# Performance work log

Measured on AMD Instinct MI355X. Metric: run time of the kernel, lower is better.

Reference implementation:

```python
import jax, jax.numpy as jnp
import numpy as np

B, C, L = 4, 256, 4096
NUM_GROUPS = 32
EPS = 1e-6


def setup_inputs() -> dict:
    key = jax.random.key(0)
    ks = jax.random.split(key, 8)
    s = 1.0 / np.sqrt(C)  # conv1x1 init scale
    return {
        "x": jax.random.normal(ks[0], (B, C, L), dtype=jnp.float32),
        "norm_g": jnp.ones((C,), dtype=jnp.float32),
        "norm_b": jnp.zeros((C,), dtype=jnp.float32),
        "q_w": jax.random.normal(ks[1], (C, C), dtype=jnp.float32) * s,
        "q_b": jnp.zeros((C,), dtype=jnp.float32),
        "k_w": jax.random.normal(ks[2], (C, C), dtype=jnp.float32) * s,
        "k_b": jnp.zeros((C,), dtype=jnp.float32),
        "v_w": jax.random.normal(ks[3], (C, C), dtype=jnp.float32) * s,
        "v_b": jnp.zeros((C,), dtype=jnp.float32),
        "proj_w": jax.random.normal(ks[4], (C, C), dtype=jnp.float32) * s,
        "proj_b": jnp.zeros((C,), dtype=jnp.float32),
    }


def _group_norm(x, g, b):
    # x: [B, C, L] -> groups of C//NUM_GROUPS channels
    Bx, Cx, Lx = x.shape
    xg = x.reshape(Bx, NUM_GROUPS, Cx // NUM_GROUPS, Lx)
    mean = jnp.mean(xg, axis=(2, 3), keepdims=True)
    var = jnp.var(xg, axis=(2, 3), keepdims=True)
    xn = ((xg - mean) * jax.lax.rsqrt(var + EPS)).reshape(Bx, Cx, Lx)
    return xn * g[None, :, None] + b[None, :, None]


def _conv1x1(w, b, h):
    # w: [Cout, Cin], h: [B, Cin, L]
    return jnp.einsum("oc,bcl->bol", w, h) + b[None, :, None]


def reference(x, norm_g, norm_b, q_w, q_b, k_w, k_b, v_w, v_b, proj_w, proj_b):
    h = _group_norm(x, norm_g, norm_b)
    q = _conv1x1(q_w, q_b, h)   # [B, C, L]
    k = _conv1x1(k_w, k_b, h)
    v = _conv1x1(v_w, v_b, h)

    scale = jnp.asarray(x.shape[1], x.dtype) ** -0.5
    # w_[b,i,j] = sum_c q[b,c,i] * k[b,c,j]
    w_ = jnp.einsum("bci,bcj->bij", q, k) * scale
    w_ = jax.nn.softmax(w_, axis=2)
    # h_[b,c,i] = sum_j v[b,c,j] * w_[b,i,j]
    h2 = jnp.einsum("bcj,bij->bci", v, w_)

    out = _conv1x1(proj_w, proj_b, h2)
    return x + out
```

## Files before the change

### kernel.cpp

```cpp
#include <hip/hip_runtime.h>

#define B_ 4
#define C_ 256
#define L_ 4096
#define NG 32
#define CPG 8
#define BL (B_ * L_)
#define KPART 4
#define KEYS_PP (L_ / KPART)
#define QLOG2E 0.09016844f

typedef __attribute__((ext_vector_type(8))) __bf16 bf16x8;
typedef __attribute__((ext_vector_type(8))) short s16x8;
typedef __attribute__((ext_vector_type(4))) float f32x4;
typedef __attribute__((ext_vector_type(16))) float f32x16;

__device__ __forceinline__ unsigned short f2bf(float f) {
  unsigned int u = __builtin_bit_cast(unsigned int, f);
  u += 0x7fffu + ((u >> 16) & 1u);
  return (unsigned short)(u >> 16);
}
__device__ __forceinline__ float bf2f(unsigned short u) {
  unsigned int v = ((unsigned int)u) << 16;
  return __builtin_bit_cast(float, v);
}
#if __has_builtin(__builtin_amdgcn_exp2f)
#define EXP2F(x) __builtin_amdgcn_exp2f(x)
#else
#define EXP2F(x) exp2f(x)
#endif

__device__ __forceinline__ void gld_lds16(const void* g, void* l) {
  __builtin_amdgcn_global_load_lds(
      (const __attribute__((address_space(1))) unsigned int*)g,
      (__attribute__((address_space(3))) unsigned int*)l, 16, 0, 0);
}

__device__ __forceinline__ float red16_add(float x) {
  int i;
  i = __builtin_amdgcn_update_dpp(0, __builtin_bit_cast(int, x), 0xB1, 0xF, 0xF, false);
  x += __builtin_bit_cast(float, i);
  i = __builtin_amdgcn_update_dpp(0, __builtin_bit_cast(int, x), 0x4E, 0xF, 0xF, false);
  x += __builtin_bit_cast(float, i);
  i = __builtin_amdgcn_update_dpp(0, __builtin_bit_cast(int, x), 0x124, 0xF, 0xF, false);
  x += __builtin_bit_cast(float, i);
  i = __builtin_amdgcn_update_dpp(0, __builtin_bit_cast(int, x), 0x128, 0xF, 0xF, false);
  x += __builtin_bit_cast(float, i);
  return x;
}

__global__ __launch_bounds__(256) void init_k(const float* __restrict__ qw,
                                              const float* __restrict__ kw,
                                              const float* __restrict__ vw,
                                              const float* __restrict__ pw,
                                              const float* __restrict__ qb,
                                              const float* __restrict__ x,
                                              unsigned short* __restrict__ wq,
                                              unsigned short* __restrict__ wk,
                                              unsigned short* __restrict__ wv,
                                              unsigned short* __restrict__ wp,
                                              float* __restrict__ qbs,
                                              float* __restrict__ stats) {
  const int bid = blockIdx.x;
  const int t = threadIdx.x;
  if (bid < 128) {
    const int m = bid >> 5;
    const int blk = bid & 31;
    const float* src = (m == 0) ? qw : (m == 1) ? kw : (m == 2) ? vw : pw;
    unsigned short* dst = (m == 0) ? wq : (m == 1) ? wk : (m == 2) ? wv : wp;
    const float sc = (m == 0) ? QLOG2E : 1.0f;
    const int base = (blk * 256 + t) * 8;
    f32x4 a = *(const f32x4*)(src + base);
    f32x4 b = *(const f32x4*)(src + base + 4);
    s16x8 o;
#pragma unroll
    for (int j = 0; j < 4; ++j) {
      o[j] = (short)f2bf(a[j] * sc);
      o[4 + j] = (short)f2bf(b[j] * sc);
    }
    *(s16x8*)(dst + base) = o;
    if (m == 0 && blk == 0) qbs[t] = qb[t] * QLOG2E;
  } else {
    const int bg = bid - 128;
    const float* base = x + (size_t)bg * (CPG * L_);
    float s = 0.f, ss = 0.f;
#pragma unroll
    for (int i = 0; i < 32; ++i) {
      f32x4 v = *(const f32x4*)(base + (size_t)(t + i * 256) * 4);
#pragma unroll
      for (int j = 0; j < 4; ++j) { s += v[j]; ss += v[j] * v[j]; }
    }
#pragma unroll
    for (int d = 1; d < 64; d <<= 1) {
      s += __shfl_xor(s, d, 64);
      ss += __shfl_xor(ss, d, 64);
    }
    __shared__ float red[8];
    if ((t & 63) == 0) { red[(t >> 6) * 2] = s; red[(t >> 6) * 2 + 1] = ss; }
    __syncthreads();
    if (t == 0) {
      float S = red[0] + red[2] + red[4] + red[6];
      float SS = red[1] + red[3] + red[5] + red[7];
      const float inv_n = 1.f / (float)(CPG * L_);
      float mean = S * inv_n;
      float var = SS * inv_n - mean * mean;
      stats[bg * 2] = mean;
      stats[bg * 2 + 1] = rsqrtf(var + 1e-6f);
    }
  }
}

__global__ __launch_bounds__(256) void gn_apply_k(const float* __restrict__ x,
                                                  const float* __restrict__ stats,
                                                  const float* __restrict__ gam,
                                                  const float* __restrict__ bet,
                                                  unsigned short* __restrict__ ht) {
  __shared__ unsigned short tile[64 * 256];
  const int blk = blockIdx.x;
  const int b = blk >> 6;
  const int l0 = (blk & 63) * 64;
  const int t = threadIdx.x;
  const int c = t;
  const float mean = stats[(b * NG + (c >> 3)) * 2];
  const float rstd = stats[(b * NG + (c >> 3)) * 2 + 1];
  const float sc = rstd * gam[c];
  const float sb = bet[c] - mean * sc;
  const float* row = x + ((size_t)(b * C_ + c)) * L_ + l0;
#pragma unroll
  for (int v = 0; v < 16; ++v) {
    f32x4 f = *(const f32x4*)(row + v * 4);
#pragma unroll
    for (int j = 0; j < 4; ++j) tile[(v * 4 + j) * 256 + c] = f2bf(f[j] * sc + sb);
  }
  __syncthreads();
#pragma unroll
  for (int i = 0; i < 8; ++i) {
    int id = t + i * 256;
    int l = id >> 5, off = id & 31;
    *(s16x8*)(ht + ((size_t)(b * L_) + l0 + l) * 256 + off * 8) =
        *(const s16x8*)(tile + l * 256 + off * 8);
  }
}

__global__ __launch_bounds__(256) void gemm_t_k(const unsigned short* __restrict__ A,
                                                const unsigned short* __restrict__ W,
                                                const float* __restrict__ bias,
                                                unsigned short* __restrict__ Ct) {
  __shared__ unsigned short Al[64 * 256];
  __shared__ unsigned short Wl[64 * 256];
  const int m0 = blockIdx.x * 64;
  const int n0 = blockIdx.y * 64;
  const int t = threadIdx.x;
  const int w = t >> 6, lane = t & 63, l15 = lane & 15, q = lane >> 4;
#pragma unroll
  for (int i = 0; i < 8; ++i) {
    const int seg = w * 8 + i;
    const int idx = seg * 64 + lane;
    const int row = idx >> 5, c16 = idx & 31;
    gld_lds16(A + (size_t)(m0 + row) * 256 + ((c16 ^ (row & 7)) * 8), Al + seg * 512);
    gld_lds16(W + (size_t)(n0 + row) * 256 + ((c16 ^ (row & 7)) * 8), Wl + seg * 512);
  }
  __syncthreads();
  bf16x8 af[8];
#pragma unroll
  for (int kf = 0; kf < 8; ++kf) {
    int row = w * 16 + l15;
    af[kf] = *(const bf16x8*)(Al + row * 256 + (((kf * 4 + q) ^ (row & 7)) * 8));
  }
  f32x4 acc[4];
#pragma unroll
  for (int nf = 0; nf < 4; ++nf) {
    f32x4 cacc = {0.f, 0.f, 0.f, 0.f};
#pragma unroll
    for (int kf = 0; kf < 8; ++kf) {
      int row = nf * 16 + l15;
      bf16x8 bf = *(const bf16x8*)(Wl + row * 256 + (((kf * 4 + q) ^ (row & 7)) * 8));
      cacc = __builtin_amdgcn_mfma_f32_16x16x32_bf16(af[kf], bf, cacc, 0, 0, 0);
    }
    acc[nf] = cacc;
  }
#pragma unroll
  for (int nf = 0; nf < 4; ++nf) {
    const int n = n0 + nf * 16 + l15;
    const float bs = bias[n];
#pragma unroll
    for (int r = 0; r < 4; ++r) {
      const int m = m0 + w * 16 + q * 4 + r;
      Ct[(size_t)m * 256 + n] = f2bf(acc[nf][r] + bs);
    }
  }
}

template <int MODE>
__global__ __launch_bounds__(256) void gemm_n_k(const unsigned short* __restrict__ X,
                                                const unsigned short* __restrict__ W,
                                                const float* __restrict__ bias,
                                                const float* __restrict__ xres,
                                                void* __restrict__ outv) {
  __shared__ unsigned short Wl[64 * 256];
  __shared__ unsigned short Xl[64 * 256];
  const int i0 = blockIdx.x * 64;
  const int o0 = blockIdx.y * 64;
  const int b = blockIdx.z;
  const int t = threadIdx.x;
  const int w = t >> 6, lane = t & 63, l15 = lane & 15, q = lane >> 4;
#pragma unroll
  for (int i = 0; i < 8; ++i) {
    const int seg = w * 8 + i;
    const int idx = seg * 64 + lane;
    const int row = idx >> 5, c16 = idx & 31;
    gld_lds16(W + (size_t)(o0 + row) * 256 + ((c16 ^ (row & 7)) * 8), Wl + seg * 512);
    gld_lds16(X + ((size_t)(b * L_) + i0 + row) * 256 + ((c16 ^ (row & 7)) * 8),
              Xl + seg * 512);
  }
  __syncthreads();
  bf16x8 af[8];
#pragma unroll
  for (int kf = 0; kf < 8; ++kf) {
    int row = w * 16 + l15;
    af[kf] = *(const bf16x8*)(Wl + row * 256 + (((kf * 4 + q) ^ (row & 7)) * 8));
  }
  f32x4 acc[4];
#pragma unroll
  for (int nf = 0; nf < 4; ++nf) {
    f32x4 cacc = {0.f, 0.f, 0.f, 0.f};
#pragma unroll
    for (int kf = 0; kf < 8; ++kf) {
      int row = nf * 16 + l15;
      bf16x8 bf = *(const bf16x8*)(Xl + row * 256 + (((kf * 4 + q) ^ (row & 7)) * 8));
      cacc = __builtin_amdgcn_mfma_f32_16x16x32_bf16(af[kf], bf, cacc, 0, 0, 0);
    }
    acc[nf] = cacc;
  }
#pragma unroll
  for (int nf = 0; nf < 4; ++nf) {
    const int i = i0 + nf * 16 + l15;
#pragma unroll
    for (int r = 0; r < 4; ++r) {
      const int o = o0 + w * 16 + q * 4 + r;
      float v = acc[nf][r] + bias[o];
      if (MODE == 0) {
        const int jt = i >> 5, jj = i & 31;
        const int qc = jj >> 3, pos = jj & 7;
        ((unsigned short*)outv)[((size_t)(b * 128 + jt)) * 8192 + o * 32 +
                                ((qc ^ ((o >> 1) & 3)) * 8) + pos] = f2bf(v);
      } else {
        const size_t idx = ((size_t)(b * C_ + o)) * L_ + i;
        ((float*)outv)[idx] = v + xres[idx];
      }
    }
  }
}

__global__ __launch_bounds__(256, 2) void attn_k(const unsigned short* __restrict__ Qt,
                                                 const unsigned short* __restrict__ Kt,
                                                 const unsigned short* __restrict__ Vg,
                                                 unsigned short* __restrict__ op01,
                                                 unsigned short* __restrict__ op23,
                                                 float* __restrict__ ml) {
  __shared__ unsigned short Kl[32 * 256];
  __shared__ unsigned short Vl[256 * 32];
  __shared__ unsigned short Pl[4 * 32 * 40];
  const int bid = blockIdx.x;
  const int g = bid & 15;
  const int b = g >> 2, part = g & 3;
  const int qi = bid >> 4;
  const int t = threadIdx.x;
  const int w = t >> 6, lane = t & 63;
  const int l15 = lane & 15, q = lane >> 4;
  const int l31 = lane & 31, h = lane >> 5;

  const int qrow0 = b * L_ + qi * 128 + w * 32;
  bf16x8 qf[2][8];
#pragma unroll
  for (int mi = 0; mi < 2; ++mi)
#pragma unroll
    for (int kf = 0; kf < 8; ++kf)
      qf[mi][kf] =
          *(const bf16x8*)(Qt + ((size_t)(qrow0 + mi * 16 + l15)) * 256 + kf * 32 + q * 8);

  f32x16 oacc[8];
#pragma unroll
  for (int nf = 0; nf < 8; ++nf)
#pragma unroll
    for (int gg = 0; gg < 16; ++gg) oacc[nf][gg] = 0.f;
  float ls0[4] = {0.f, 0.f, 0.f, 0.f}, ls1[4] = {0.f, 0.f, 0.f, 0.f};

  const unsigned short* kbase = Kt + ((size_t)(b * L_ + part * KEYS_PP)) * 256;
  const unsigned short* vbase = Vg + ((size_t)(b * 128 + part * 32)) * 8192;
  unsigned short* Pw = Pl + w * 1280;

  for (int it = 0; it < KEYS_PP / 32; ++it) {
    __syncthreads();
    {
      const unsigned short* ksrc = kbase + (size_t)(it * 32) * 256;
      const unsigned short* vsrc = vbase + (size_t)it * 8192;
#pragma unroll
      for (int i = 0; i < 4; ++i) {
        const int seg = w * 4 + i;
        const int idx = seg * 64 + lane;
        const int row = idx >> 5, c16 = idx & 31;
        gld_lds16(ksrc + (size_t)row * 256 + ((c16 ^ (row & 7)) * 8), Kl + seg * 512);
        gld_lds16(vsrc + (size_t)idx * 8, Vl + seg * 512);
      }
    }
    __syncthreads();

    f32x4 s00 = {0.f, 0.f, 0.f, 0.f}, s01 = s00, s10 = s00, s11 = s00;
#pragma unroll
    for (int kf = 0; kf < 8; ++kf) {
      const int ch = ((kf * 4 + q) ^ (l15 & 7)) * 8;
      bf16x8 kb0 = *(const bf16x8*)(Kl + l15 * 256 + ch);
      bf16x8 kb1 = *(const bf16x8*)(Kl + (16 + l15) * 256 + ch);
      s00 = __builtin_amdgcn_mfma_f32_16x16x32_bf16(qf[0][kf], kb0, s00, 0, 0, 0);
      s01 = __builtin_amdgcn_mfma_f32_16x16x32_bf16(qf[0][kf], kb1, s01, 0, 0, 0);
      s10 = __builtin_amdgcn_mfma_f32_16x16x32_bf16(qf[1][kf], kb0, s10, 0, 0, 0);
      s11 = __builtin_amdgcn_mfma_f32_16x16x32_bf16(qf[1][kf], kb1, s11, 0, 0, 0);
    }
#pragma unroll
    for (int r = 0; r < 4; ++r) {
      float p00 = EXP2F(s00[r]), p01 = EXP2F(s01[r]);
      float p10 = EXP2F(s10[r]), p11 = EXP2F(s11[r]);
      ls0[r] += p00 + p01;
      ls1[r] += p10 + p11;
      Pw[(q * 4 + r) * 40 + l15] = f2bf(p00);
      Pw[(q * 4 + r) * 40 + 16 + l15] = f2bf(p01);
      Pw[(16 + q * 4 + r) * 40 + l15] = f2bf(p10);
      Pw[(16 + q * 4 + r) * 40 + 16 + l15] = f2bf(p11);
    }
    bf16x8 pa0 = *(const bf16x8*)(Pw + l31 * 40 + h * 8);
    bf16x8 pa1 = *(const bf16x8*)(Pw + l31 * 40 + 16 + h * 8);
#pragma unroll
    for (int nf = 0; nf < 8; ++nf) {
      const int c = nf * 32 + l31;
      bf16x8 v0 = *(const bf16x8*)(Vl + c * 32 + ((h ^ ((c >> 1) & 3)) * 8));
      bf16x8 v1 = *(const bf16x8*)(Vl + c * 32 + (((2 + h) ^ ((c >> 1) & 3)) * 8));
      oacc[nf] = __builtin_amdgcn_mfma_f32_32x32x16_bf16(pa0, v0, oacc[nf], 0, 0, 0);
      oacc[nf] = __builtin_amdgcn_mfma_f32_32x32x16_bf16(pa1, v1, oacc[nf], 0, 0, 0);
    }
  }

  unsigned short* opb = (part < 2) ? op01 + (size_t)part * BL * 256
                                   : op23 + (size_t)(part - 2) * BL * 256;
#pragma unroll
  for (int nf = 0; nf < 8; ++nf)
#pragma unroll
    for (int gg = 0; gg < 16; ++gg) {
      const int row = (gg & 3) + 8 * (gg >> 2) + 4 * h;
      opb[(size_t)(qrow0 + row) * 256 + nf * 32 + l31] = f2bf(oacc[nf][gg]);
    }
#pragma unroll
  for (int r = 0; r < 4; ++r) {
    ls0[r] = red16_add(ls0[r]);
    ls1[r] = red16_add(ls1[r]);
  }
  if (l15 == 0) {
    float* mlp = ml + (size_t)part * BL;
#pragma unroll
    for (int r = 0; r < 4; ++r) {
      mlp[qrow0 + q * 4 + r] = ls0[r];
      mlp[qrow0 + 16 + q * 4 + r] = ls1[r];
    }
  }
}

__global__ __launch_bounds__(256) void merge_k(const unsigned short* __restrict__ op01,
                                               const unsigned short* __restrict__ op23,
                                               const float* __restrict__ ml,
                                               unsigned short* __restrict__ Om) {
  const int row = blockIdx.x * 8 + (threadIdx.x >> 5);
  const int c8 = threadIdx.x & 31;
  const float inv = 1.0f / (ml[row] + ml[BL + row] + ml[2 * BL + row] + ml[3 * BL + row]);
  const size_t off = (size_t)row * 256 + c8 * 8;
  s16x8 v0 = *(const s16x8*)(op01 + off);
  s16x8 v1 = *(const s16x8*)(op01 + (size_t)BL * 256 + off);
  s16x8 v2 = *(const s16x8*)(op23 + off);
  s16x8 v3 = *(const s16x8*)(op23 + (size_t)BL * 256 + off);
  s16x8 o;
#pragma unroll
  for (int j = 0; j < 8; ++j)
    o[j] = (short)f2bf((bf2f((unsigned short)v0[j]) + bf2f((unsigned short)v1[j]) +
                        bf2f((unsigned short)v2[j]) + bf2f((unsigned short)v3[j])) *
                       inv);
  *(s16x8*)(Om + off) = o;
}

extern "C" void kernel_launch(void* const* d_in, const int* in_sizes, int n_in,
                              void* d_out, int out_size, void* d_ws, size_t ws_size,
                              hipStream_t stream) {
  const float* x = (const float*)d_in[0];
  const float* norm_g = (const float*)d_in[1];
  const float* norm_b = (const float*)d_in[2];
  const float* q_w = (const float*)d_in[3];
  const float* q_b = (const float*)d_in[4];
  const float* k_w = (const float*)d_in[5];
  const float* k_b = (const float*)d_in[6];
  const float* v_w = (const float*)d_in[7];
  const float* v_b = (const float*)d_in[8];
  const float* p_w = (const float*)d_in[9];
  const float* p_b = (const float*)d_in[10];
  float* out = (float*)d_out;
  (void)in_sizes; (void)n_in; (void)out_size; (void)ws_size;

  char* ws = (char*)d_ws;
  const size_t MB = 1u << 20;
  float* stats = (float*)ws;
  float* qbs = (float*)(ws + 1024);
  unsigned short* wq = (unsigned short*)(ws + 4096);
  unsigned short* wk = wq + 65536;
  unsigned short* wv = wk + 65536;
  unsigned short* wp = wv + 65536;
  unsigned short* ht = (unsigned short*)(ws + 1 * MB);
  unsigned short* qt = (unsigned short*)(ws + 9 * MB);
  unsigned short* kt = (unsigned short*)(ws + 17 * MB);
  unsigned short* vg = (unsigned short*)(ws + 25 * MB);
  unsigned short* op23 = (unsigned short*)(ws + 33 * MB);
  float* ml = (float*)(ws + 50 * MB);
  unsigned short* op01 = (unsigned short*)d_out;

  init_k<<<256, 256, 0, stream>>>(q_w, k_w, v_w, p_w, q_b, x, wq, wk, wv, wp, qbs, stats);
  gn_apply_k<<<B_ * (L_ / 64), 256, 0, stream>>>(x, stats, norm_g, norm_b, ht);
  gemm_t_k<<<dim3((B_ * L_) / 64, C_ / 64), 256, 0, stream>>>(ht, wq, qbs, qt);
  gemm_t_k<<<dim3((B_ * L_) / 64, C_ / 64), 256, 0, stream>>>(ht, wk, k_b, kt);
  gemm_n_k<0><<<dim3(L_ / 64, C_ / 64, B_), 256, 0, stream>>>(ht, wv, v_b, nullptr, vg);
  attn_k<<<512, 256, 0, stream>>>(qt, kt, vg, op01, op23, ml);
  merge_k<<<BL / 8, 256, 0, stream>>>(op01, op23, ml, ht);
  gemm_n_k<1><<<dim3(L_ / 64, C_ / 64, B_), 256, 0, stream>>>(ht, wp, p_b, x, out);
}
```

Measured before the change: 209.5 us.

## Fuse Q/K/V projections into one launch and split PV across waves by channel

Merges the three separate Q, K and V projection GEMM launches into one grid using blockIdx.z to pick the weight, bias and output layout. This removes two kernel launches and their tail effects. In the attention kernel, the P·V stage now waits on a block barrier and has each wave own 64 channels across all four waves' 32-query P tiles, instead of each wave covering all 256 channels for its own queries. That cuts per-wave V fragment loads from LDS and keeps V in registers across the query tiles, at the cost of an extra __syncthreads per key tile and a different output store pattern.

```diff
diff --git a/kernel.cpp b/kernel.cpp
--- a/kernel.cpp
+++ b/kernel.cpp
@@ -142,12 +142,21 @@
   }
 }
 
-__global__ __launch_bounds__(256) void gemm_t_k(const unsigned short* __restrict__ A,
-                                                const unsigned short* __restrict__ W,
-                                                const float* __restrict__ bias,
-                                                unsigned short* __restrict__ Ct) {
+__global__ __launch_bounds__(256) void qkv_k(const unsigned short* __restrict__ ht,
+                                             const unsigned short* __restrict__ wq,
+                                             const unsigned short* __restrict__ wk,
+                                             const unsigned short* __restrict__ wv,
+                                             const float* __restrict__ qbs,
+                                             const float* __restrict__ kbias,
+                                             const float* __restrict__ vbias,
+                                             unsigned short* __restrict__ qt,
+                                             unsigned short* __restrict__ kt,
+                                             unsigned short* __restrict__ vg) {
   __shared__ unsigned short Al[64 * 256];
   __shared__ unsigned short Wl[64 * 256];
+  const int z = blockIdx.z;
+  const unsigned short* W = (z == 0) ? wq : (z == 1) ? wk : wv;
+  const float* bias = (z == 0) ? qbs : (z == 1) ? kbias : vbias;
   const int m0 = blockIdx.x * 64;
   const int n0 = blockIdx.y * 64;
   const int t = threadIdx.x;
@@ -157,7 +166,7 @@
     const int seg = w * 8 + i;
     const int idx = seg * 64 + lane;
     const int row = idx >> 5, c16 = idx & 31;
-    gld_lds16(A + (size_t)(m0 + row) * 256 + ((c16 ^ (row & 7)) * 8), Al + seg * 512);
+    gld_lds16(ht + (size_t)(m0 + row) * 256 + ((c16 ^ (row & 7)) * 8), Al + seg * 512);
     gld_lds16(W + (size_t)(n0 + row) * 256 + ((c16 ^ (row & 7)) * 8), Wl + seg * 512);
   }
   __syncthreads();
@@ -179,6 +188,7 @@
     }
     acc[nf] = cacc;
   }
+  unsigned short* Ct = (z == 0) ? qt : kt;
 #pragma unroll
   for (int nf = 0; nf < 4; ++nf) {
     const int n = n0 + nf * 16 + l15;
@@ -186,17 +196,25 @@
 #pragma unroll
     for (int r = 0; r < 4; ++r) {
       const int m = m0 + w * 16 + q * 4 + r;
-      Ct[(size_t)m * 256 + n] = f2bf(acc[nf][r] + bs);
-    }
-  }
-}
-
-template <int MODE>
-__global__ __launch_bounds__(256) void gemm_n_k(const unsigned short* __restrict__ X,
-                                                const unsigned short* __restrict__ W,
-                                                const float* __restrict__ bias,
-                                                const float* __restrict__ xres,
-                                                void* __restrict__ outv) {
+      const float v = acc[nf][r] + bs;
+      if (z < 2) {
+        Ct[(size_t)m * 256 + n] = f2bf(v);
+      } else {
+        const int b = m >> 12, i = m & (L_ - 1);
+        const int jt = i >> 5, jj = i & 31;
+        const int qc = jj >> 3, pos = jj & 7;
+        vg[((size_t)(b * 128 + jt)) * 8192 + n * 32 + ((qc ^ ((n >> 1) & 3)) * 8) + pos] =
+            f2bf(v);
+      }
+    }
+  }
+}
+
+__global__ __launch_bounds__(256) void proj_k(const unsigned short* __restrict__ X,
+                                              const unsigned short* __restrict__ W,
+                                              const float* __restrict__ bias,
+                                              const float* __restrict__ xres,
+                                              float* __restrict__ out) {
   __shared__ unsigned short Wl[64 * 256];
   __shared__ unsigned short Xl[64 * 256];
   const int i0 = blockIdx.x * 64;
@@ -238,16 +256,8 @@
 #pragma unroll
     for (int r = 0; r < 4; ++r) {
       const int o = o0 + w * 16 + q * 4 + r;
-      float v = acc[nf][r] + bias[o];
-      if (MODE == 0) {
-        const int jt = i >> 5, jj = i & 31;
-        const int qc = jj >> 3, pos = jj & 7;
-        ((unsigned short*)outv)[((size_t)(b * 128 + jt)) * 8192 + o * 32 +
-                                ((qc ^ ((o >> 1) & 3)) * 8) + pos] = f2bf(v);
-      } else {
-        const size_t idx = ((size_t)(b * C_ + o)) * L_ + i;
-        ((float*)outv)[idx] = v + xres[idx];
-      }
+      const size_t idx = ((size_t)(b * C_ + o)) * L_ + i;
+      out[idx] = acc[nf][r] + bias[o] + xres[idx];
     }
   }
 }
@@ -328,27 +338,44 @@
       Pw[(16 + q * 4 + r) * 40 + l15] = f2bf(p10);
       Pw[(16 + q * 4 + r) * 40 + 16 + l15] = f2bf(p11);
     }
-    bf16x8 pa0 = *(const bf16x8*)(Pw + l31 * 40 + h * 8);
-    bf16x8 pa1 = *(const bf16x8*)(Pw + l31 * 40 + 16 + h * 8);
-#pragma unroll
-    for (int nf = 0; nf < 8; ++nf) {
-      const int c = nf * 32 + l31;
-      bf16x8 v0 = *(const bf16x8*)(Vl + c * 32 + ((h ^ ((c >> 1) & 3)) * 8));
-      bf16x8 v1 = *(const bf16x8*)(Vl + c * 32 + (((2 + h) ^ ((c >> 1) & 3)) * 8));
-      oacc[nf] = __builtin_amdgcn_mfma_f32_32x32x16_bf16(pa0, v0, oacc[nf], 0, 0, 0);
-      oacc[nf] = __builtin_amdgcn_mfma_f32_32x32x16_bf16(pa1, v1, oacc[nf], 0, 0, 0);
+    __syncthreads();
+
+    bf16x8 va[2][2];
+#pragma unroll
+    for (int nf = 0; nf < 2; ++nf) {
+      const int c = w * 64 + nf * 32 + l31;
+#pragma unroll
+      for (int kc = 0; kc < 2; ++kc)
+        va[nf][kc] =
+            *(const bf16x8*)(Vl + c * 32 + (((kc * 2 + h) ^ ((c >> 1) & 3)) * 8));
+    }
+#pragma unroll
+    for (int qt2 = 0; qt2 < 4; ++qt2) {
+      bf16x8 pa0 = *(const bf16x8*)(Pl + qt2 * 1280 + l31 * 40 + h * 8);
+      bf16x8 pa1 = *(const bf16x8*)(Pl + qt2 * 1280 + l31 * 40 + 16 + h * 8);
+#pragma unroll
+      for (int nf = 0; nf < 2; ++nf) {
+        oacc[qt2 * 2 + nf] =
+            __builtin_amdgcn_mfma_f32_32x32x16_bf16(pa0, va[nf][0], oacc[qt2 * 2 + nf], 0, 0, 0);
+        oacc[qt2 * 2 + nf] =
+            __builtin_amdgcn_mfma_f32_32x32x16_bf16(pa1, va[nf][1], oacc[qt2 * 2 + nf], 0, 0, 0);
+      }
     }
   }
 
   unsigned short* opb = (part < 2) ? op01 + (size_t)part * BL * 256
                                    : op23 + (size_t)(part - 2) * BL * 256;
-#pragma unroll
-  for (int nf = 0; nf < 8; ++nf)
-#pragma unroll
-    for (int gg = 0; gg < 16; ++gg) {
-      const int row = (gg & 3) + 8 * (gg >> 2) + 4 * h;
-      opb[(size_t)(qrow0 + row) * 256 + nf * 32 + l31] = f2bf(oacc[nf][gg]);
-    }
+  const int qb0 = b * L_ + qi * 128;
+#pragma unroll
+  for (int qt2 = 0; qt2 < 4; ++qt2)
+#pragma unroll
+    for (int nf = 0; nf < 2; ++nf)
+#pragma unroll
+      for (int gg = 0; gg < 16; ++gg) {
+        const int row = qt2 * 32 + (gg & 3) + 8 * (gg >> 2) + 4 * h;
+        opb[(size_t)(qb0 + row) * 256 + w * 64 + nf * 32 + l31] =
+            f2bf(oacc[qt2 * 2 + nf][gg]);
+      }
 #pragma unroll
   for (int r = 0; r < 4; ++r) {
     ls0[r] = red16_add(ls0[r]);
@@ -420,10 +447,9 @@
 
   init_k<<<256, 256, 0, stream>>>(q_w, k_w, v_w, p_w, q_b, x, wq, wk, wv, wp, qbs, stats);
   gn_apply_k<<<B_ * (L_ / 64), 256, 0, stream>>>(x, stats, norm_g, norm_b, ht);
-  gemm_t_k<<<dim3((B_ * L_) / 64, C_ / 64), 256, 0, stream>>>(ht, wq, qbs, qt);
-  gemm_t_k<<<dim3((B_ * L_) / 64, C_ / 64), 256, 0, stream>>>(ht, wk, k_b, kt);
-  gemm_n_k<0><<<dim3(L_ / 64, C_ / 64, B_), 256, 0, stream>>>(ht, wv, v_b, nullptr, vg);
+  qkv_k<<<dim3((B_ * L_) / 64, C_ / 64, 3), 256, 0, stream>>>(ht, wq, wk, wv, qbs, k_b,
+                                                              v_b, qt, kt, vg);
   attn_k<<<512, 256, 0, stream>>>(qt, kt, vg, op01, op23, ml);
   merge_k<<<BL / 8, 256, 0, stream>>>(op01, op23, ml, ht);
-  gemm_n_k<1><<<dim3(L_ / 64, C_ / 64, B_), 256, 0, stream>>>(ht, wp, p_b, x, out);
-}
+  proj_k<<<dim3(L_ / 64, C_ / 64, B_), 256, 0, stream>>>(ht, wp, p_b, x, out);
+}
```

Result: slower. 223.4 us (+6.6%).
